# Kernel optimization log

Hardware: AMD Instinct MI355X
Metric: run time of the kernel (lower is better)

## Reference

```python
import jax, jax.numpy as jnp
import numpy as np

DIM = 1024
N_HEADS = 16
HEAD_DIM = DIM // N_HEADS
HIDDEN = 4 * DIM
B, T = 4, 2048
EPS = 1e-5


def setup_inputs() -> dict:
    key = jax.random.key(0)
    ks = jax.random.split(key, 12)
    s = lambda fan_in: 1.0 / np.sqrt(fan_in)
    return {
        "x": jax.random.normal(ks[0], (B, T, DIM), jnp.float32),
        "ln1_g": jnp.ones((DIM,), jnp.float32),
        "ln1_b": jnp.zeros((DIM,), jnp.float32),
        "qkv_w": jax.random.normal(ks[1], (DIM, 3 * DIM), jnp.float32) * s(DIM),
        "qkv_b": jnp.zeros((3 * DIM,), jnp.float32),
        "proj_w": jax.random.normal(ks[2], (DIM, DIM), jnp.float32) * s(DIM),
        "proj_b": jnp.zeros((DIM,), jnp.float32),
        "ln2_g": jnp.ones((DIM,), jnp.float32),
        "ln2_b": jnp.zeros((DIM,), jnp.float32),
        "ff1_w": jax.random.normal(ks[3], (DIM, HIDDEN), jnp.float32) * s(DIM),
        "ff1_b": jnp.zeros((HIDDEN,), jnp.float32),
        "ff2_w": jax.random.normal(ks[4], (HIDDEN, DIM), jnp.float32) * s(HIDDEN),
        "ff2_b": jnp.zeros((DIM,), jnp.float32),
    }


def _layernorm(x, g, b):
    mu = jnp.mean(x, axis=-1, keepdims=True)
    var = jnp.mean(jnp.square(x - mu), axis=-1, keepdims=True)
    return (x - mu) * jax.lax.rsqrt(var + EPS) * g + b


def _attn(x, qkv_w, qkv_b, proj_w, proj_b):
    Bx, Tx, C = x.shape
    qkv = (x @ qkv_w + qkv_b).reshape(Bx, Tx, 3, N_HEADS, HEAD_DIM)
    q, k, v = (qkv[:, :, i].transpose(0, 2, 1, 3) for i in range(3))  # [B,H,T,hd]
    att = jnp.einsum('bhqd,bhkd->bhqk', q, k) / np.sqrt(HEAD_DIM)
    causal = jnp.tril(jnp.ones((Tx, Tx), bool))
    att = jnp.where(causal, att, -jnp.inf)
    att = jax.nn.softmax(att, axis=-1)
    out = jnp.einsum('bhqk,bhkd->bhqd', att, v).transpose(0, 2, 1, 3).reshape(Bx, Tx, C)
    return out @ proj_w + proj_b


def reference(x, ln1_g, ln1_b, qkv_w, qkv_b, proj_w, proj_b,
              ln2_g, ln2_b, ff1_w, ff1_b, ff2_w, ff2_b):
    x = x + _attn(_layernorm(x, ln1_g, ln1_b), qkv_w, qkv_b, proj_w, proj_b)
    h = _layernorm(x, ln2_g, ln2_b)
    h = jax.nn.gelu(h @ ff1_w + ff1_b, approximate=False) @ ff2_w + ff2_b
    return x + h
```

## Files before the change

### kernel.cpp

```cpp
#include <hip/hip_runtime.h>
#include <hip/hip_bf16.h>
#include <math.h>

#define DIM 1024
#define NHEADS 16
#define HD 64
#define TT 2048
#define BB 4
#define MTOK (BB*TT)
#define HID 4096

typedef __attribute__((ext_vector_type(8))) short bf16x8;
typedef __attribute__((ext_vector_type(4))) float f32x4;
typedef unsigned short u16;
typedef unsigned int u32;

__device__ inline u16 f2b(float f){
  __hip_bfloat16 h = __float2bfloat16(f);
  return __builtin_bit_cast(u16, h);
}

__device__ inline u32 cvtpk(float lo, float hi_){
  u32 r;
  asm("v_cvt_pk_bf16_f32 %0, %1, %2" : "=v"(r) : "v"(lo), "v"(hi_));
  return r;
}

__device__ inline void load_lds16(const void* g, void* l){
  __builtin_amdgcn_global_load_lds(
      (const __attribute__((address_space(1))) void*)g,
      (__attribute__((address_space(3))) void*)l,
      16, 0, 0);
}

__global__ __launch_bounds__(256) void wconv_t(const float* __restrict__ W,
                                               u16* __restrict__ Wt, int K, int N){
  __shared__ float tl[32][33];
  const int k0 = blockIdx.x*32, n0 = blockIdx.y*32;
  const int tx = threadIdx.x & 31, ty = threadIdx.x >> 5;
  #pragma unroll
  for (int r=0;r<32;r+=8)
    tl[ty+r][tx] = W[(size_t)(k0+ty+r)*N + (n0+tx)];
  __syncthreads();
  #pragma unroll
  for (int r=0;r<32;r+=8)
    Wt[(size_t)(n0+ty+r)*K + (k0+tx)] = f2b(tl[tx][ty+r]);
}

__global__ __launch_bounds__(256) void ln_fwd(const float* __restrict__ x,
                                              const float* __restrict__ g,
                                              const float* __restrict__ bta,
                                              u16* __restrict__ out){
  const int row = blockIdx.x, t = threadIdx.x;
  const float4 v = ((const float4*)(x + (size_t)row*DIM))[t];
  float s  = v.x+v.y+v.z+v.w;
  float s2 = v.x*v.x+v.y*v.y+v.z*v.z+v.w*v.w;
  #pragma unroll
  for (int m=1;m<64;m<<=1){ s += __shfl_xor(s,m); s2 += __shfl_xor(s2,m); }
  __shared__ float red[8];
  if ((t&63)==0){ red[t>>6]=s; red[4+(t>>6)]=s2; }
  __syncthreads();
  s  = red[0]+red[1]+red[2]+red[3];
  s2 = red[4]+red[5]+red[6]+red[7];
  const float mu = s*(1.0f/DIM);
  const float rstd = rsqrtf(s2*(1.0f/DIM) - mu*mu + 1e-5f);
  const float4 gv = ((const float4*)g)[t];
  const float4 bv = ((const float4*)bta)[t];
  ushort4 ov;
  ov.x = f2b((v.x-mu)*rstd*gv.x + bv.x);
  ov.y = f2b((v.y-mu)*rstd*gv.y + bv.y);
  ov.z = f2b((v.z-mu)*rstd*gv.z + bv.z);
  ov.w = f2b((v.w-mu)*rstd*gv.w + bv.w);
  ((ushort4*)out)[(size_t)row*(DIM/4) + t] = ov;
}

template<int EPI, bool DBUF>
__global__ __launch_bounds__(256) void gemm_bt(
    const u16* __restrict__ A, const u16* __restrict__ Bt,
    const float* __restrict__ bias, const float* __restrict__ resid,
    float* __restrict__ outf, u16* __restrict__ outh,
    u16* __restrict__ qo, u16* __restrict__ ko, u16* __restrict__ vo,
    int M, int N, int K)
{
  __shared__ __align__(16) u16 smem[DBUF ? 32768 : 16384];
  u16* Ct = smem;
  const int t = threadIdx.x, wv = t>>6, ln = t&63;
  const int nbx = gridDim.x, nwg = nbx*gridDim.y;
  const int bid = blockIdx.y*nbx + blockIdx.x;
  const int cpx = nwg>>3;
  const int wid = (bid&7)*cpx + (bid>>3);
  const int m0 = (wid/nbx)*128, n0 = (wid%nbx)*128;
  const int wr = wv>>1, wc = wv&1;
  const int hi = ln>>4, lr = hi*4, lc = ln&15;
  f32x4 acc[4][4] = {};

  int rdoff[2];
  #pragma unroll
  for (int kk=0; kk<2; kk++)
    rdoff[kk] = ((kk*4 + hi) ^ (lc&7)) << 3;

  auto STAGE = [&](int buf, int kt){
    u16* As = smem + buf*16384;
    u16* Bs = smem + buf*16384 + 8192;
    #pragma unroll
    for (int j=0;j<4;j++){
      const int chunk = j*256 + t;
      const int row = chunk>>3;
      const int cS  = (chunk&7) ^ (row&7);
      load_lds16(A  + (size_t)(m0+row)*K + kt + cS*8, (char*)As + chunk*16);
      load_lds16(Bt + (size_t)(n0+row)*K + kt + cS*8, (char*)Bs + chunk*16);
    }
  };
  auto COMPUTE = [&](int buf){
    const u16* As = smem + buf*16384;
    const u16* Bs = smem + buf*16384 + 8192;
    bf16x8 af[4][2], bfr[4][2];
    #pragma unroll
    for (int mi=0;mi<4;mi++){
      const int rbase = (wr*64 + mi*16 + lc) << 6;
      af[mi][0] = *(const bf16x8*)&As[rbase + rdoff[0]];
      af[mi][1] = *(const bf16x8*)&As[rbase + rdoff[1]];
    }
    #pragma unroll
    for (int ni=0;ni<4;ni++){
      const int rbase = (wc*64 + ni*16 + lc) << 6;
      bfr[ni][0] = *(const bf16x8*)&Bs[rbase + rdoff[0]];
      bfr[ni][1] = *(const bf16x8*)&Bs[rbase + rdoff[1]];
    }
    #pragma unroll
    for (int kk=0;kk<2;kk++)
      #pragma unroll
      for (int mi=0;mi<4;mi++)
        #pragma unroll
        for (int ni=0;ni<4;ni++)
          acc[mi][ni] = __builtin_amdgcn_mfma_f32_16x16x32_bf16(af[mi][kk], bfr[ni][kk], acc[mi][ni], 0,0,0);
  };

  if constexpr (DBUF){
    STAGE(0, 0);
    asm volatile("s_waitcnt vmcnt(0)" ::: "memory");
    __syncthreads();
    int cur = 0;
    for (int kt=64; kt<K; kt+=64){
      STAGE(cur^1, kt);
      COMPUTE(cur);
      asm volatile("s_waitcnt vmcnt(0)" ::: "memory");
      __syncthreads();
      cur ^= 1;
    }
    COMPUTE(cur);
  } else {
    for (int kt=0; kt<K; kt+=64){
      STAGE(0, kt);
      asm volatile("s_waitcnt vmcnt(0)" ::: "memory");
      __syncthreads();
      COMPUTE(0);
      __syncthreads();
    }
  }

  if constexpr (EPI==1 || EPI==3){
    #pragma unroll
    for (int ni=0;ni<4;ni++){
      const int gn = n0 + wc*64 + ni*16 + lc;
      const float bv = bias[gn];
      #pragma unroll
      for (int mi=0;mi<4;mi++){
        const int gmb = m0 + wr*64 + mi*16 + lr;
        f32x4 a = acc[mi][ni];
        #pragma unroll
        for (int i=0;i<4;i++){
          const size_t idx = (size_t)(gmb+i)*DIM + gn;
          outf[idx] = a[i] + bv + resid[idx];
        }
      }
    }
  } else {
    const int part = (EPI==0) ? (n0>>10) : 0;
    __syncthreads();
    #pragma unroll
    for (int ni=0;ni<4;ni++){
      const int gn = n0 + wc*64 + ni*16 + lc;
      const float bv = bias[gn];
      const int cl = wc*64 + ni*16 + lc;
      #pragma unroll
      for (int mi=0;mi<4;mi++){
        f32x4 a = acc[mi][ni];
        #pragma unroll
        for (int i=0;i<4;i++){
          const int rl = wr*64 + mi*16 + lr + i;
          float val = a[i] + bv;
          if constexpr (EPI==2){
            const float xx = val*val;
            const float w  = val * fmaf(xx, 0.10294322f, 2.30220781f);
            const float y  = exp2f(w);
            const float r_ = __builtin_amdgcn_rcpf(1.0f + y);
            val = val - val*r_;
          }
          int r = rl, c = cl;
          if (EPI==0 && part==2){ r = cl; c = rl; }
          const int chunk = c>>3;
          const int csw = (chunk&8) | ((chunk ^ (r&7)) & 7);
          Ct[(r<<7) + (csw<<3) + (c&7)] = f2b(val);
        }
      }
    }
    __syncthreads();
    const int cid = t & 7, rsub = t >> 3;
    const int bb = m0>>11, tok0b = m0&2047;
    const int h0 = (EPI==0) ? ((n0&1023)>>6) : 0;
    #pragma unroll
    for (int pass=0; pass<4; ++pass){
      const int rr = pass*32 + rsub;
      #pragma unroll
      for (int hh=0; hh<2; ++hh){
        const int chunk = hh*8 + cid;
        const int sw = (chunk&8) | ((chunk ^ (rr&7)) & 7);
        const bf16x8 vvv = *(const bf16x8*)&Ct[(rr<<7) + (sw<<3)];
        if constexpr (EPI==2){
          *(bf16x8*)&outh[(size_t)(m0+rr)*HID + n0 + chunk*8] = vvv;
        } else {
          if (part==2){
            const int head = h0 + (rr>>6), d = rr&63;
            *(bf16x8*)&vo[(((size_t)bb*NHEADS + head)*HD + d)*TT + tok0b + chunk*8] = vvv;
          } else {
            u16* dst = part ? ko : qo;
            const int head = h0 + hh;
            *(bf16x8*)&dst[(((size_t)bb*NHEADS + head)*TT + tok0b + rr)*HD + cid*8] = vvv;
          }
        }
      }
    }
  }
}

__global__ __launch_bounds__(512) void attn_fwd(
    const u16* __restrict__ qpt, const u16* __restrict__ kb, const u16* __restrict__ vtb,
    u16* __restrict__ o)
{
  __shared__ __align__(16) u16 Kd[2][64*64];
  __shared__ __align__(16) u16 Vd[2][64*64];
  const int t = threadIdx.x, wv = t>>6, ln = t&63;
  const int bid  = blockIdx.y*gridDim.x + blockIdx.x;
  const int orig = (bid&7)*64 + (bid>>3);
  const int bh   = orig>>3;
  const int qp   = orig&7;
  const int qbA  = qp, qbB = 15-qp;
  const size_t base = (size_t)bh*TT*HD;
  const int hi = ln>>4, lc = ln&15;
  const int ntA = 2*qbA + 2, ntB = 2*qbB + 2;
  const int qbaseA = qbA*128 + wv*16, qrowA = qbaseA + lc;
  const int qbaseB = qbB*128 + wv*16, qrowB = qbaseB + lc;

  const bf16x8 qfA0 = *(const bf16x8*)(qpt + base + (size_t)qrowA*HD + hi*8);
  const bf16x8 qfA1 = *(const bf16x8*)(qpt + base + (size_t)qrowA*HD + 32 + hi*8);
  const bf16x8 qfB0 = *(const bf16x8*)(qpt + base + (size_t)qrowB*HD + hi*8);
  const bf16x8 qfB1 = *(const bf16x8*)(qpt + base + (size_t)qrowB*HD + 32 + hi*8);
  f32x4 oaccA[4] = {}, oaccB[4] = {};
  f32x4 lsumA = {0.f,0.f,0.f,0.f}, lsumB = {0.f,0.f,0.f,0.f};
  float mrunA = -1e30f, mrunB = -1e30f;
  const float SCQ = 0.125f * 1.44269504f;
  bf16x8 ones;
  #pragma unroll
  for (int j=0;j<8;j++) ones[j] = (short)0x3F80;

  const int srow = t>>3;
  const int sch  = t&7;
  const int gch  = (sch ^ (srow&7))<<3;

  auto STAGE = [&](int nb, int kt){
    load_lds16(kb  + base + (size_t)(kt*64+srow)*HD + gch, &Kd[nb][srow*64 + sch*8]);
    load_lds16(vtb + base + (size_t)srow*TT + kt*64 + gch, &Vd[nb][srow*64 + sch*8]);
  };
  auto FRAG = [&](const u16* buf, int r, int ch)->bf16x8{
    return *(const bf16x8*)(buf + r*64 + ((ch ^ (r&7))<<3));
  };
  const int src0 = ((ln&16)<<1) + lc;
  const int src1 = src0 + 16;
  auto pick = [&](u32 w0, u32 w1, int src)->u32{
    const u32 a = (u32)__shfl((int)w0, src);
    const u32 b = (u32)__shfl((int)w1, src);
    return (hi<2) ? a : b;
  };

  auto strip_tile = [&](int kt, const u16* Kb, const u16* Vb,
                        const bf16x8& qf0, const bf16x8& qf1,
                        int qbase, int qrow,
                        f32x4* oacc, f32x4& lsum, float& mrun){
    if (kt*64 > qbase + 15) return;
    float sv[4][4];
    __builtin_amdgcn_s_setprio(1);
    #pragma unroll
    for (int cf=0;cf<4;cf++){
      const int r = cf*16 + lc;
      const bf16x8 kf0 = FRAG(Kb, r, hi);
      const bf16x8 kf1 = FRAG(Kb, r, hi+4);
      f32x4 z = {0.f,0.f,0.f,0.f};
      z = __builtin_amdgcn_mfma_f32_16x16x32_bf16(kf0, qf0, z, 0,0,0);
      z = __builtin_amdgcn_mfma_f32_16x16x32_bf16(kf1, qf1, z, 0,0,0);
      sv[cf][0]=z[0]; sv[cf][1]=z[1]; sv[cf][2]=z[2]; sv[cf][3]=z[3];
    }
    __builtin_amdgcn_s_setprio(0);
    float mx = -1e30f;
    if (kt*64 + 63 > qbase){
      #pragma unroll
      for (int cf=0;cf<4;cf++)
        #pragma unroll
        for (int i=0;i<4;i++){
          const int kvg = kt*64 + cf*16 + 4*hi + i;
          float s_ = sv[cf][i]*SCQ;
          s_ = (kvg > qrow) ? -1e30f : s_;
          sv[cf][i] = s_;
          mx = fmaxf(mx, s_);
        }
    } else {
      #pragma unroll
      for (int cf=0;cf<4;cf++)
        #pragma unroll
        for (int i=0;i<4;i++){
          const float s_ = sv[cf][i]*SCQ;
          sv[cf][i] = s_;
          mx = fmaxf(mx, s_);
        }
    }
    mx = fmaxf(mx, __shfl_xor(mx, 16));
    mx = fmaxf(mx, __shfl_xor(mx, 32));
    if (__any(mx > mrun + 11.0f)){
      const float mnew = fmaxf(mrun, mx);
      const float sc = exp2f(mrun - mnew);
      mrun = mnew;
      const float s0 = __shfl(sc, 4*hi+0);
      const float s1 = __shfl(sc, 4*hi+1);
      const float s2 = __shfl(sc, 4*hi+2);
      const float s3 = __shfl(sc, 4*hi+3);
      #pragma unroll
      for (int df=0;df<4;df++){
        oacc[df][0] *= s0; oacc[df][1] *= s1;
        oacc[df][2] *= s2; oacc[df][3] *= s3;
      }
      lsum[0] *= s0; lsum[1] *= s1; lsum[2] *= s2; lsum[3] *= s3;
    }
    u32 W[4][2];
    #pragma unroll
    for (int cf=0;cf<4;cf++){
      const float e0 = exp2f(sv[cf][0] - mrun);
      const float e1 = exp2f(sv[cf][1] - mrun);
      const float e2 = exp2f(sv[cf][2] - mrun);
      const float e3 = exp2f(sv[cf][3] - mrun);
      W[cf][0] = cvtpk(e0, e1);
      W[cf][1] = cvtpk(e2, e3);
    }
    uint4 uA, uB;
    uA.x = pick(W[0][0], W[1][0], src0);
    uA.y = pick(W[0][1], W[1][1], src0);
    uA.z = pick(W[0][0], W[1][0], src1);
    uA.w = pick(W[0][1], W[1][1], src1);
    uB.x = pick(W[2][0], W[3][0], src0);
    uB.y = pick(W[2][1], W[3][1], src0);
    uB.z = pick(W[2][0], W[3][0], src1);
    uB.w = pick(W[2][1], W[3][1], src1);
    const bf16x8 paA = __builtin_bit_cast(bf16x8, uA);
    const bf16x8 paB = __builtin_bit_cast(bf16x8, uB);
    __builtin_amdgcn_s_setprio(1);
    #pragma unroll
    for (int df=0;df<4;df++){
      const bf16x8 v0 = FRAG(Vb, df*16+lc, hi);
      const bf16x8 v1 = FRAG(Vb, df*16+lc, hi+4);
      oacc[df] = __builtin_amdgcn_mfma_f32_16x16x32_bf16(paA, v0, oacc[df], 0,0,0);
      oacc[df] = __builtin_amdgcn_mfma_f32_16x16x32_bf16(paB, v1, oacc[df], 0,0,0);
    }
    lsum = __builtin_amdgcn_mfma_f32_16x16x32_bf16(paA, ones, lsum, 0,0,0);
    lsum = __builtin_amdgcn_mfma_f32_16x16x32_bf16(paB, ones, lsum, 0,0,0);
    __builtin_amdgcn_s_setprio(0);
  };

  int cur = 0;
  STAGE(0, 0);
  asm volatile("s_waitcnt vmcnt(0)" ::: "memory");
  __syncthreads();

  for (int kt=0; kt<ntB; kt++){
    if (kt+1 < ntB) STAGE(cur^1, kt+1);
    const u16* Kb = Kd[cur];
    const u16* Vb = Vd[cur];
    strip_tile(kt, Kb, Vb, qfB0, qfB1, qbaseB, qrowB, oaccB, lsumB, mrunB);
    if (kt < ntA)
      strip_tile(kt, Kb, Vb, qfA0, qfA1, qbaseA, qrowA, oaccA, lsumA, mrunA);
    asm volatile("s_waitcnt vmcnt(0)" ::: "memory");
    __syncthreads();
    cur ^= 1;
  }

  const int b = bh>>4, h = bh&15;
  {
    const float inv[4] = {1.0f/lsumA[0], 1.0f/lsumA[1], 1.0f/lsumA[2], 1.0f/lsumA[3]};
    const int qg0 = qbaseA + 4*hi;
    #pragma unroll
    for (int i=0;i<4;i++){
      const size_t rowb = ((size_t)b*TT + (size_t)(qg0 + i))*DIM + h*HD;
      #pragma unroll
      for (int df=0;df<4;df++)
        o[rowb + df*16 + lc] = f2b(oaccA[df][i]*inv[i]);
    }
  }
  {
    const float inv[4] = {1.0f/lsumB[0], 1.0f/lsumB[1], 1.0f/lsumB[2], 1.0f/lsumB[3]};
    const int qg0 = qbaseB + 4*hi;
    #pragma unroll
    for (int i=0;i<4;i++){
      const size_t rowb = ((size_t)b*TT + (size_t)(qg0 + i))*DIM + h*HD;
      #pragma unroll
      for (int df=0;df<4;df++)
        o[rowb + df*16 + lc] = f2b(oaccB[df][i]*inv[i]);
    }
  }
}

extern "C" void kernel_launch(void* const* d_in, const int* in_sizes, int n_in,
                              void* d_out, int out_size, void* d_ws, size_t ws_size,
                              hipStream_t stream){
  (void)in_sizes; (void)n_in; (void)out_size; (void)ws_size;
  const float* x     = (const float*)d_in[0];
  const float* ln1g  = (const float*)d_in[1];
  const float* ln1b  = (const float*)d_in[2];
  const float* qkvw  = (const float*)d_in[3];
  const float* qkvb  = (const float*)d_in[4];
  const float* projw = (const float*)d_in[5];
  const float* projb = (const float*)d_in[6];
  const float* ln2g  = (const float*)d_in[7];
  const float* ln2b  = (const float*)d_in[8];
  const float* ff1w  = (const float*)d_in[9];
  const float* ff1b  = (const float*)d_in[10];
  const float* ff2w  = (const float*)d_in[11];
  const float* ff2b  = (const float*)d_in[12];
  float* out = (float*)d_out;

  char* ws = (char*)d_ws;
  size_t off = 0;
  auto alloc = [&](size_t n){ char* p = ws + off; off += (n + 255) & ~(size_t)255; return p; };
  u16* wqkvt  = (u16*)alloc((size_t)3072*1024*2);
  u16* wprojt = (u16*)alloc((size_t)1024*1024*2);
  u16* wff1t  = (u16*)alloc((size_t)4096*1024*2);
  u16* wff2t  = (u16*)alloc((size_t)1024*4096*2);
  u16* h1     = (u16*)alloc((size_t)MTOK*DIM*2);
  u16* qbuf   = (u16*)alloc((size_t)MTOK*DIM*2);
  u16* kbuf   = (u16*)alloc((size_t)MTOK*DIM*2);
  u16* vbuf   = (u16*)alloc((size_t)MTOK*DIM*2);
  u16* aout   = (u16*)alloc((size_t)MTOK*DIM*2);
  float* x2   = (float*)alloc((size_t)MTOK*DIM*4);
  u16* h2     = (u16*)alloc((size_t)MTOK*DIM*2);
  u16* act    = (u16*)alloc((size_t)MTOK*HID*2);

  wconv_t<<<dim3(1024/32, 3072/32), 256, 0, stream>>>(qkvw, wqkvt, 1024, 3072);
  wconv_t<<<dim3(1024/32, 1024/32), 256, 0, stream>>>(projw, wprojt, 1024, 1024);
  wconv_t<<<dim3(1024/32, 4096/32), 256, 0, stream>>>(ff1w, wff1t, 1024, 4096);
  wconv_t<<<dim3(4096/32, 1024/32), 256, 0, stream>>>(ff2w, wff2t, 4096, 1024);

  ln_fwd<<<MTOK, 256, 0, stream>>>(x, ln1g, ln1b, h1);

  gemm_bt<0,false><<<dim3(3072/128, MTOK/128), 256, 0, stream>>>(
      h1, wqkvt, qkvb, nullptr, nullptr, nullptr, qbuf, kbuf, vbuf, MTOK, 3072, 1024);

  attn_fwd<<<dim3(8, BB*NHEADS), 512, 0, stream>>>(qbuf, kbuf, vbuf, aout);

  gemm_bt<1,true><<<dim3(1024/128, MTOK/128), 256, 0, stream>>>(
      aout, wprojt, projb, x, x2, nullptr, nullptr, nullptr, nullptr, MTOK, 1024, 1024);

  ln_fwd<<<MTOK, 256, 0, stream>>>(x2, ln2g, ln2b, h2);

  gemm_bt<2,false><<<dim3(4096/128, MTOK/128), 256, 0, stream>>>(
      h2, wff1t, ff1b, nullptr, nullptr, act, nullptr, nullptr, nullptr, MTOK, HID, 1024);

  gemm_bt<3,true><<<dim3(1024/128, MTOK/128), 256, 0, stream>>>(
      act, wff2t, ff2b, x2, out, nullptr, nullptr, nullptr, nullptr, MTOK, DIM, HID);
}
```

Before: 422.9 us.

## Add 256x256-tile double-buffered GEMM for QKV and FF1 projections

Introduces a new 512-thread GEMM kernel with 256x256 output tiles, 128KB dynamic LDS double buffering, swizzled LDS layout and split staging interleaved with MFMA phases. It replaces the 128x128 single-buffered gemm_bt for the QKV and FF1 matmuls, falling back to the old kernel if the large-LDS attribute cannot be set. The intent is higher arithmetic intensity per tile and overlap of global loads with compute. In exchange it uses far more LDS and registers per workgroup, which lowers occupancy, and it launches fewer workgroups (192 for QKV, 256 for FF1), so tail effects can matter.

Measured after the change: 462.3 us. +9.3%, slower.

```diff
diff --git a/kernel.cpp b/kernel.cpp
--- a/kernel.cpp
+++ b/kernel.cpp
@@ -74,6 +74,154 @@
   ((ushort4*)out)[(size_t)row*(DIM/4) + t] = ov;
 }
 
+template<int EPI>
+__global__ __launch_bounds__(512, 2) void gemm256(
+    const u16* __restrict__ A, const u16* __restrict__ Bt,
+    const float* __restrict__ bias, u16* __restrict__ outh,
+    u16* __restrict__ qo, u16* __restrict__ ko, u16* __restrict__ vo,
+    int K)
+{
+  extern __shared__ __align__(16) u16 smem[];
+  u16* Ct = smem;
+  const int t = threadIdx.x, wv = t>>6, ln = t&63;
+  const int nbx = gridDim.x, nwg = nbx*gridDim.y;
+  const int bid = blockIdx.y*nbx + blockIdx.x;
+  const int cpx = nwg>>3;
+  const int wid = (bid&7)*cpx + (bid>>3);
+  const int m0 = (wid/nbx)*256, n0 = (wid%nbx)*256;
+  const int wr = wv>>2, wc = wv&3;
+  const int hi = ln>>4, lc = ln&15;
+  f32x4 acc[8][4] = {};
+
+  auto slot = [&](int par, int which, int kk)->u16*{
+    return smem + (((par<<1)|which)*2 + kk)*8192;
+  };
+  auto STAGE = [&](int par, int kt, int which, int kk){
+    const u16* src = which ? Bt : A;
+    const int org = which ? n0 : m0;
+    u16* dst = slot(par, which, kk);
+    #pragma unroll
+    for (int j=0;j<2;j++){
+      const int id = j*512 + t;
+      const int row = id>>2, c = id&3;
+      const int cs = c ^ ((row>>1)&3);
+      load_lds16(src + (size_t)(org+row)*K + kt*64 + kk*32 + cs*8, dst + id*8);
+    }
+  };
+  auto RD = [&](const u16* base, int r)->bf16x8{
+    return *(const bf16x8*)(base + r*32 + ((hi ^ ((r>>1)&3))<<3));
+  };
+
+  const int nkt = K>>6;
+  STAGE(0,0,0,0); STAGE(0,0,1,0); STAGE(0,0,0,1); STAGE(0,0,1,1);
+
+  for (int tt=0; tt<nkt; ++tt){
+    const int par = tt&1;
+    const bool st = (tt+1) < nkt;
+    #pragma unroll
+    for (int kk=0; kk<2; ++kk){
+      if (!st && kk==1) asm volatile("s_waitcnt vmcnt(0)" ::: "memory");
+      else              asm volatile("s_waitcnt vmcnt(4)" ::: "memory");
+      __builtin_amdgcn_s_barrier();
+      const u16* As_ = slot(par,0,kk);
+      const u16* Bs_ = slot(par,1,kk);
+      bf16x8 af[8];
+      #pragma unroll
+      for (int mi=0;mi<8;mi++) af[mi] = RD(As_, wr*128 + mi*16 + lc);
+      bf16x8 b0 = RD(Bs_, wc*64 + lc);
+      bf16x8 b1 = RD(Bs_, wc*64 + 16 + lc);
+      if (st) STAGE(par^1, tt+1, 0, kk);
+      asm volatile("s_waitcnt lgkmcnt(0)" ::: "memory");
+      __builtin_amdgcn_sched_barrier(0);
+      __builtin_amdgcn_s_setprio(1);
+      #pragma unroll
+      for (int mi=0;mi<8;mi++){
+        acc[mi][0] = __builtin_amdgcn_mfma_f32_16x16x32_bf16(af[mi], b0, acc[mi][0], 0,0,0);
+        acc[mi][1] = __builtin_amdgcn_mfma_f32_16x16x32_bf16(af[mi], b1, acc[mi][1], 0,0,0);
+      }
+      __builtin_amdgcn_s_setprio(0);
+      __builtin_amdgcn_s_barrier();
+      bf16x8 b2 = RD(Bs_, wc*64 + 32 + lc);
+      bf16x8 b3 = RD(Bs_, wc*64 + 48 + lc);
+      if (st) STAGE(par^1, tt+1, 1, kk);
+      asm volatile("s_waitcnt lgkmcnt(0)" ::: "memory");
+      __builtin_amdgcn_sched_barrier(0);
+      __builtin_amdgcn_s_setprio(1);
+      #pragma unroll
+      for (int mi=0;mi<8;mi++){
+        acc[mi][2] = __builtin_amdgcn_mfma_f32_16x16x32_bf16(af[mi], b2, acc[mi][2], 0,0,0);
+        acc[mi][3] = __builtin_amdgcn_mfma_f32_16x16x32_bf16(af[mi], b3, acc[mi][3], 0,0,0);
+      }
+      __builtin_amdgcn_s_setprio(0);
+    }
+  }
+  __syncthreads();
+
+  const int bb = m0>>11;
+  #pragma unroll
+  for (int h=0;h<2;h++){
+    #pragma unroll
+    for (int ch=0;ch<2;ch++){
+      const int part = (EPI==0) ? ((n0 + ch*128)>>10) : 0;
+      const int h0 = ((n0 + ch*128)&1023)>>6;
+      __syncthreads();
+      if (wr==h && (wc>>1)==ch){
+        #pragma unroll
+        for (int ni=0;ni<4;ni++){
+          const int gn = n0 + wc*64 + ni*16 + lc;
+          const float bv = bias[gn];
+          const int cl = (wc&1)*64 + ni*16 + lc;
+          #pragma unroll
+          for (int mi=0;mi<8;mi++){
+            f32x4 a = acc[mi][ni];
+            #pragma unroll
+            for (int i=0;i<4;i++){
+              const int rl = mi*16 + hi*4 + i;
+              float val = a[i] + bv;
+              if constexpr (EPI==2){
+                const float xx = val*val;
+                const float w  = val * fmaf(xx, 0.10294322f, 2.30220781f);
+                const float y  = exp2f(w);
+                const float r_ = __builtin_amdgcn_rcpf(1.0f + y);
+                val = val - val*r_;
+              }
+              int r = rl, c = cl;
+              if (EPI==0 && part==2){ r = cl; c = rl; }
+              const int chunk = c>>3;
+              const int csw = (chunk&8) | ((chunk ^ (r&7)) & 7);
+              Ct[(r<<7) + (csw<<3) + (c&7)] = f2b(val);
+            }
+          }
+        }
+      }
+      __syncthreads();
+      const int cid = t&7, rsub = t>>3;
+      const int tok0b = (m0&2047) + h*128;
+      #pragma unroll
+      for (int p2=0;p2<2;p2++){
+        const int rr = p2*64 + rsub;
+        #pragma unroll
+        for (int hh=0;hh<2;hh++){
+          const int chunk = hh*8 + cid;
+          const int sw = (chunk&8) | ((chunk ^ (rr&7)) & 7);
+          const bf16x8 vvv = *(const bf16x8*)&Ct[(rr<<7) + (sw<<3)];
+          if constexpr (EPI==2){
+            *(bf16x8*)&outh[(size_t)(m0 + h*128 + rr)*HID + n0 + ch*128 + chunk*8] = vvv;
+          } else {
+            if (part==2){
+              const int head = h0 + (rr>>6), d = rr&63;
+              *(bf16x8*)&vo[(((size_t)bb*NHEADS + head)*HD + d)*TT + tok0b + chunk*8] = vvv;
+            } else {
+              u16* dst = part ? ko : qo;
+              *(bf16x8*)&dst[(((size_t)bb*NHEADS + h0 + hh)*TT + tok0b + rr)*HD + cid*8] = vvv;
+            }
+          }
+        }
+      }
+    }
+  }
+}
+
 template<int EPI, bool DBUF>
 __global__ __launch_bounds__(256) void gemm_bt(
     const u16* __restrict__ A, const u16* __restrict__ Bt,
@@ -451,6 +599,12 @@
   u16* h2     = (u16*)alloc((size_t)MTOK*DIM*2);
   u16* act    = (u16*)alloc((size_t)MTOK*HID*2);
 
+  hipError_t eA = hipFuncSetAttribute(reinterpret_cast<const void*>(&gemm256<0>),
+                                      hipFuncAttributeMaxDynamicSharedMemorySize, 131072);
+  hipError_t eB = hipFuncSetAttribute(reinterpret_cast<const void*>(&gemm256<2>),
+                                      hipFuncAttributeMaxDynamicSharedMemorySize, 131072);
+  const bool big = (eA == hipSuccess) && (eB == hipSuccess);
+
   wconv_t<<<dim3(1024/32, 3072/32), 256, 0, stream>>>(qkvw, wqkvt, 1024, 3072);
   wconv_t<<<dim3(1024/32, 1024/32), 256, 0, stream>>>(projw, wprojt, 1024, 1024);
   wconv_t<<<dim3(1024/32, 4096/32), 256, 0, stream>>>(ff1w, wff1t, 1024, 4096);
@@ -458,8 +612,12 @@
 
   ln_fwd<<<MTOK, 256, 0, stream>>>(x, ln1g, ln1b, h1);
 
-  gemm_bt<0,false><<<dim3(3072/128, MTOK/128), 256, 0, stream>>>(
-      h1, wqkvt, qkvb, nullptr, nullptr, nullptr, qbuf, kbuf, vbuf, MTOK, 3072, 1024);
+  if (big)
+    gemm256<0><<<dim3(3072/256, MTOK/256), 512, 131072, stream>>>(
+        h1, wqkvt, qkvb, nullptr, qbuf, kbuf, vbuf, 1024);
+  else
+    gemm_bt<0,false><<<dim3(3072/128, MTOK/128), 256, 0, stream>>>(
+        h1, wqkvt, qkvb, nullptr, nullptr, nullptr, qbuf, kbuf, vbuf, MTOK, 3072, 1024);
 
   attn_fwd<<<dim3(8, BB*NHEADS), 512, 0, stream>>>(qbuf, kbuf, vbuf, aout);
 
@@ -468,8 +626,12 @@
 
   ln_fwd<<<MTOK, 256, 0, stream>>>(x2, ln2g, ln2b, h2);
 
-  gemm_bt<2,false><<<dim3(4096/128, MTOK/128), 256, 0, stream>>>(
-      h2, wff1t, ff1b, nullptr, nullptr, act, nullptr, nullptr, nullptr, MTOK, HID, 1024);
+  if (big)
+    gemm256<2><<<dim3(4096/256, MTOK/256), 512, 131072, stream>>>(
+        h2, wff1t, ff1b, act, nullptr, nullptr, nullptr, 1024);
+  else
+    gemm_bt<2,false><<<dim3(4096/128, MTOK/128), 256, 0, stream>>>(
+        h2, wff1t, ff1b, nullptr, nullptr, act, nullptr, nullptr, nullptr, MTOK, HID, 1024);
 
   gemm_bt<3,true><<<dim3(1024/128, MTOK/128), 256, 0, stream>>>(
       act, wff2t, ff2b, x2, out, nullptr, nullptr, nullptr, nullptr, MTOK, DIM, HID);
```

## Add triple-buffered BK=32 GEMM pipeline for QKV and FF1 projections

Applied to the files above, without the earlier changes.

Replaces the single-buffered BK=64 main loop used by the QKV and FF1 GEMMs with a three-stage LDS ring of BK=32 tiles. Loads run two tiles ahead and are tracked with partial vmcnt waits, so the loop needs one barrier per step instead of two. It also raises wave priority around the MFMA block. The aim is to hide global-to-LDS latency behind matrix math. In exchange it uses 48KB of LDS instead of 32KB, which may lower occupancy, and it halves the MFMA work per barrier.

Measured after the change: 416.0 us. About the same (-1.6%).

```diff
diff --git a/kernel.cpp b/kernel.cpp
--- a/kernel.cpp
+++ b/kernel.cpp
@@ -74,7 +74,7 @@
   ((ushort4*)out)[(size_t)row*(DIM/4) + t] = ov;
 }
 
-template<int EPI, bool DBUF>
+template<int EPI, int MODE>
 __global__ __launch_bounds__(256) void gemm_bt(
     const u16* __restrict__ A, const u16* __restrict__ Bt,
     const float* __restrict__ bias, const float* __restrict__ resid,
@@ -82,7 +82,7 @@
     u16* __restrict__ qo, u16* __restrict__ ko, u16* __restrict__ vo,
     int M, int N, int K)
 {
-  __shared__ __align__(16) u16 smem[DBUF ? 32768 : 16384];
+  __shared__ __align__(16) u16 smem[MODE==2 ? 24576 : 32768];
   u16* Ct = smem;
   const int t = threadIdx.x, wv = t>>6, ln = t&63;
   const int nbx = gridDim.x, nwg = nbx*gridDim.y;
@@ -94,49 +94,93 @@
   const int hi = ln>>4, lr = hi*4, lc = ln&15;
   f32x4 acc[4][4] = {};
 
-  int rdoff[2];
-  #pragma unroll
-  for (int kk=0; kk<2; kk++)
-    rdoff[kk] = ((kk*4 + hi) ^ (lc&7)) << 3;
-
-  auto STAGE = [&](int buf, int kt){
-    u16* As = smem + buf*16384;
-    u16* Bs = smem + buf*16384 + 8192;
-    #pragma unroll
-    for (int j=0;j<4;j++){
-      const int chunk = j*256 + t;
-      const int row = chunk>>3;
-      const int cS  = (chunk&7) ^ (row&7);
-      load_lds16(A  + (size_t)(m0+row)*K + kt + cS*8, (char*)As + chunk*16);
-      load_lds16(Bt + (size_t)(n0+row)*K + kt + cS*8, (char*)Bs + chunk*16);
-    }
-  };
-  auto COMPUTE = [&](int buf){
-    const u16* As = smem + buf*16384;
-    const u16* Bs = smem + buf*16384 + 8192;
-    bf16x8 af[4][2], bfr[4][2];
-    #pragma unroll
-    for (int mi=0;mi<4;mi++){
-      const int rbase = (wr*64 + mi*16 + lc) << 6;
-      af[mi][0] = *(const bf16x8*)&As[rbase + rdoff[0]];
-      af[mi][1] = *(const bf16x8*)&As[rbase + rdoff[1]];
-    }
-    #pragma unroll
-    for (int ni=0;ni<4;ni++){
-      const int rbase = (wc*64 + ni*16 + lc) << 6;
-      bfr[ni][0] = *(const bf16x8*)&Bs[rbase + rdoff[0]];
-      bfr[ni][1] = *(const bf16x8*)&Bs[rbase + rdoff[1]];
-    }
-    #pragma unroll
-    for (int kk=0;kk<2;kk++)
+  if constexpr (MODE==2){
+    auto STAGE32 = [&](int buf, int kt){
+      u16* As = smem + buf*8192;
+      u16* Bs = smem + buf*8192 + 4096;
+      #pragma unroll
+      for (int j=0;j<2;j++){
+        const int id = j*256 + t;
+        const int row = id>>2, c = id&3;
+        const int cs = c ^ ((row>>1)&3);
+        load_lds16(A  + (size_t)(m0+row)*K + kt + cs*8, (char*)As + id*16);
+        load_lds16(Bt + (size_t)(n0+row)*K + kt + cs*8, (char*)Bs + id*16);
+      }
+    };
+    auto RD32 = [&](const u16* base, int r)->bf16x8{
+      return *(const bf16x8*)(base + r*32 + ((hi ^ ((r>>1)&3))<<3));
+    };
+    auto COMPUTE32 = [&](int buf){
+      const u16* As = smem + buf*8192;
+      const u16* Bs = smem + buf*8192 + 4096;
+      bf16x8 af[4], bfr[4];
+      #pragma unroll
+      for (int mi=0;mi<4;mi++) af[mi] = RD32(As, wr*64 + mi*16 + lc);
+      #pragma unroll
+      for (int ni=0;ni<4;ni++) bfr[ni] = RD32(Bs, wc*64 + ni*16 + lc);
+      __builtin_amdgcn_s_setprio(1);
       #pragma unroll
       for (int mi=0;mi<4;mi++)
         #pragma unroll
         for (int ni=0;ni<4;ni++)
-          acc[mi][ni] = __builtin_amdgcn_mfma_f32_16x16x32_bf16(af[mi][kk], bfr[ni][kk], acc[mi][ni], 0,0,0);
-  };
-
-  if constexpr (DBUF){
+          acc[mi][ni] = __builtin_amdgcn_mfma_f32_16x16x32_bf16(af[mi], bfr[ni], acc[mi][ni], 0,0,0);
+      __builtin_amdgcn_s_setprio(0);
+    };
+    const int nk = K>>5;
+    STAGE32(0, 0);
+    STAGE32(1, 32);
+    asm volatile("s_waitcnt vmcnt(4)" ::: "memory");
+    __builtin_amdgcn_s_barrier();
+    for (int tt=0; tt<nk; ++tt){
+      if (tt+2 < nk) STAGE32((tt+2)%3, (tt+2)<<5);
+      COMPUTE32(tt%3);
+      if (tt+1 < nk){
+        if (tt+2 < nk) asm volatile("s_waitcnt vmcnt(4)" ::: "memory");
+        else           asm volatile("s_waitcnt vmcnt(0)" ::: "memory");
+        __builtin_amdgcn_s_barrier();
+      }
+    }
+  } else {
+    int rdoff[2];
+    #pragma unroll
+    for (int kk=0; kk<2; kk++)
+      rdoff[kk] = ((kk*4 + hi) ^ (lc&7)) << 3;
+    auto STAGE = [&](int buf, int kt){
+      u16* As = smem + buf*16384;
+      u16* Bs = smem + buf*16384 + 8192;
+      #pragma unroll
+      for (int j=0;j<4;j++){
+        const int chunk = j*256 + t;
+        const int row = chunk>>3;
+        const int cS  = (chunk&7) ^ (row&7);
+        load_lds16(A  + (size_t)(m0+row)*K + kt + cS*8, (char*)As + chunk*16);
+        load_lds16(Bt + (size_t)(n0+row)*K + kt + cS*8, (char*)Bs + chunk*16);
+      }
+    };
+    auto COMPUTE = [&](int buf){
+      const u16* As = smem + buf*16384;
+      const u16* Bs = smem + buf*16384 + 8192;
+      bf16x8 af[4][2], bfr[4][2];
+      #pragma unroll
+      for (int mi=0;mi<4;mi++){
+        const int rbase = (wr*64 + mi*16 + lc) << 6;
+        af[mi][0] = *(const bf16x8*)&As[rbase + rdoff[0]];
+        af[mi][1] = *(const bf16x8*)&As[rbase + rdoff[1]];
+      }
+      #pragma unroll
+      for (int ni=0;ni<4;ni++){
+        const int rbase = (wc*64 + ni*16 + lc) << 6;
+        bfr[ni][0] = *(const bf16x8*)&Bs[rbase + rdoff[0]];
+        bfr[ni][1] = *(const bf16x8*)&Bs[rbase + rdoff[1]];
+      }
+      #pragma unroll
+      for (int kk=0;kk<2;kk++)
+        #pragma unroll
+        for (int mi=0;mi<4;mi++)
+          #pragma unroll
+          for (int ni=0;ni<4;ni++)
+            acc[mi][ni] = __builtin_amdgcn_mfma_f32_16x16x32_bf16(af[mi][kk], bfr[ni][kk], acc[mi][ni], 0,0,0);
+    };
     STAGE(0, 0);
     asm volatile("s_waitcnt vmcnt(0)" ::: "memory");
     __syncthreads();
@@ -149,14 +193,6 @@
       cur ^= 1;
     }
     COMPUTE(cur);
-  } else {
-    for (int kt=0; kt<K; kt+=64){
-      STAGE(0, kt);
-      asm volatile("s_waitcnt vmcnt(0)" ::: "memory");
-      __syncthreads();
-      COMPUTE(0);
-      __syncthreads();
-    }
   }
 
   if constexpr (EPI==1 || EPI==3){
@@ -458,19 +494,19 @@
 
   ln_fwd<<<MTOK, 256, 0, stream>>>(x, ln1g, ln1b, h1);
 
-  gemm_bt<0,false><<<dim3(3072/128, MTOK/128), 256, 0, stream>>>(
+  gemm_bt<0,2><<<dim3(3072/128, MTOK/128), 256, 0, stream>>>(
       h1, wqkvt, qkvb, nullptr, nullptr, nullptr, qbuf, kbuf, vbuf, MTOK, 3072, 1024);
 
   attn_fwd<<<dim3(8, BB*NHEADS), 512, 0, stream>>>(qbuf, kbuf, vbuf, aout);
 
-  gemm_bt<1,true><<<dim3(1024/128, MTOK/128), 256, 0, stream>>>(
+  gemm_bt<1,1><<<dim3(1024/128, MTOK/128), 256, 0, stream>>>(
       aout, wprojt, projb, x, x2, nullptr, nullptr, nullptr, nullptr, MTOK, 1024, 1024);
 
   ln_fwd<<<MTOK, 256, 0, stream>>>(x2, ln2g, ln2b, h2);
 
-  gemm_bt<2,false><<<dim3(4096/128, MTOK/128), 256, 0, stream>>>(
+  gemm_bt<2,2><<<dim3(4096/128, MTOK/128), 256, 0, stream>>>(
       h2, wff1t, ff1b, nullptr, nullptr, act, nullptr, nullptr, nullptr, MTOK, HID, 1024);
 
-  gemm_bt<3,true><<<dim3(1024/128, MTOK/128), 256, 0, stream>>>(
+  gemm_bt<3,1><<<dim3(1024/128, MTOK/128), 256, 0, stream>>>(
       act, wff2t, ff2b, x2, out, nullptr, nullptr, nullptr, nullptr, MTOK, DIM, HID);
 }
```
